# Kernel tuning notes

Hardware: AMD Instinct MI355X
Metric: run time of the kernel (lower is better)

Reference implementation:

```python
import jax, jax.numpy as jnp
import numpy as np

EPS = 1e-5

def _layernorm(x, w, b):
    mu = jnp.mean(x, axis=-1, keepdims=True)
    var = jnp.mean(jnp.square(x - mu), axis=-1, keepdims=True)
    return (x - mu) * jax.lax.rsqrt(var + EPS) * w + b

def setup_inputs() -> dict:
    key = jax.random.key(0)
    ks = jax.random.split(key, 8)
    L, D, FF = 4096, 768, 3072
    s = 1.0 / np.sqrt(D)
    return {
        "x": jax.random.normal(ks[0], (L, D), jnp.float32),
        "in_proj_w": jax.random.normal(ks[1], (3 * D, D), jnp.float32) * s,
        "in_proj_b": jnp.zeros((3 * D,), jnp.float32),
        "out_w": jax.random.normal(ks[2], (D, D), jnp.float32) * s,
        "out_b": jnp.zeros((D,), jnp.float32),
        "ln1_w": jnp.ones((D,), jnp.float32),
        "ln1_b": jnp.zeros((D,), jnp.float32),
        "ln2_w": jnp.ones((D,), jnp.float32),
        "ln2_b": jnp.zeros((D,), jnp.float32),
        "ff_w1": jax.random.normal(ks[3], (FF, D), jnp.float32) * s,
        "ff_b1": jnp.zeros((FF,), jnp.float32),
        "ff_w2": jax.random.normal(ks[4], (D, FF), jnp.float32) * (1.0 / np.sqrt(FF)),
        "ff_b2": jnp.zeros((D,), jnp.float32),
        "window": 128,
    }

def reference(x, in_proj_w, in_proj_b, out_w, out_b, ln1_w, ln1_b, ln2_w, ln2_b, ff_w1, ff_b1, ff_w2, ff_b2, window):
    L, D = x.shape
    H = 12
    hd = D // H
    # packed qkv projection (torch MultiheadAttention in_proj)
    qkv = x @ in_proj_w.T + in_proj_b          # [L, 3D]
    q, k, v = jnp.split(qkv, 3, axis=-1)
    q = q.reshape(L, H, hd).transpose(1, 0, 2)  # [H, L, hd]
    k = k.reshape(L, H, hd).transpose(1, 0, 2)
    v = v.reshape(L, H, hd).transpose(1, 0, 2)
    scores = jnp.einsum('hqd,hkd->hqk', q, k) / np.sqrt(hd)  # [H, L, L]
    idx = jnp.arange(L)
    banned = jnp.abs(idx[:, None] - idx[None, :]) > window    # True = disallowed
    scores = jnp.where(banned[None], -jnp.inf, scores)
    probs = jax.nn.softmax(scores, axis=-1)
    ctx = jnp.einsum('hqk,hkd->hqd', probs, v)               # [H, L, hd]
    ctx = ctx.transpose(1, 0, 2).reshape(L, D)
    attn_out = ctx @ out_w.T + out_b
    h = _layernorm(x + attn_out, ln1_w, ln1_b)
    ff = jax.nn.gelu(h @ ff_w1.T + ff_b1, approximate=False) @ ff_w2.T + ff_b2
    return _layernorm(h + ff, ln2_w, ln2_b)
```

## Files before the change

### kernel.cpp

```cpp
#include <hip/hip_runtime.h>

typedef __bf16 bf16x8 __attribute__((ext_vector_type(8)));
typedef float f32x4 __attribute__((ext_vector_type(4)));

__device__ __forceinline__ unsigned short f2b(float f) {
    unsigned int u = __float_as_uint(f);
    u = (u + 0x7fffu + ((u >> 16) & 1u)) >> 16;
    return (unsigned short)u;
}
__device__ __forceinline__ float b2f(unsigned short v) {
    return __uint_as_float(((unsigned int)v) << 16);
}

__global__ __launch_bounds__(256) void cvt_all(
    const float* __restrict__ s0, unsigned short* __restrict__ d0,
    const float* __restrict__ s1, unsigned short* __restrict__ d1,
    const float* __restrict__ s2, unsigned short* __restrict__ d2,
    const float* __restrict__ s3, unsigned short* __restrict__ d3,
    const float* __restrict__ s4, unsigned short* __restrict__ d4)
{
    int i = blockIdx.x * 256 + threadIdx.x;
    const float* s; unsigned short* d; int j;
    if (i < 786432)       { s = s0; d = d0; j = i; }
    else if (i < 1228800) { s = s1; d = d1; j = i - 786432; }
    else if (i < 1376256) { s = s2; d = d2; j = i - 1228800; }
    else if (i < 1966080) { s = s3; d = d3; j = i - 1376256; }
    else                  { s = s4; d = d4; j = i - 1966080; }
    float4 v = ((const float4*)s)[j];
    ushort4 o;
    o.x = f2b(v.x); o.y = f2b(v.y); o.z = f2b(v.z); o.w = f2b(v.w);
    ((ushort4*)d)[j] = o;
}

#define GL16(g, s) __builtin_amdgcn_global_load_lds( \
    (const __attribute__((address_space(1))) unsigned int*)(g), \
    (__attribute__((address_space(3))) unsigned int*)(s), 16, 0, 0)

template<int EPI>
__global__ __launch_bounds__(256) void gemm128(
    const unsigned short* __restrict__ A,
    const unsigned short* __restrict__ B,
    const float* __restrict__ bias,
    unsigned short* __restrict__ Cb,
    int M, int N, int K)
{
    __shared__ __align__(16) unsigned short As[128 * 64];
    __shared__ __align__(16) unsigned short Bs[128 * 64];
    const int nwg = gridDim.x * gridDim.y;
    const int lin = blockIdx.y * gridDim.x + blockIdx.x;
    const int qq = nwg >> 3;
    const int swz = (lin & 7) * qq + (lin >> 3);
    const int bx = swz % gridDim.x;
    const int by = swz / gridDim.x;

    const int tid = threadIdx.x;
    const int l = tid & 63;
    const int w = tid >> 6;
    const int wr = w >> 1, wc = w & 1;
    const long arow = (long)by * 128 + (tid >> 3);
    const long brow = (long)bx * 128 + (tid >> 3);
    const int kc = (tid & 7) * 8;
    const unsigned short* Ap = A + arow * K + kc;
    const unsigned short* Bp = B + brow * K + kc;

    const int kslice = K / gridDim.z;
    const int kbeg = blockIdx.z * kslice;
    const int kend = kbeg + kslice;

    f32x4 acc[4][4] = {};

    for (int k0 = kbeg; k0 < kend; k0 += 64) {
#pragma unroll
        for (int i = 0; i < 4; ++i) {
            GL16(Ap + k0 + (long)32 * i * K, As + i * 2048 + tid * 8);
            GL16(Bp + k0 + (long)32 * i * K, Bs + i * 2048 + tid * 8);
        }
        __syncthreads();
#pragma unroll
        for (int kk = 0; kk < 2; ++kk) {
            bf16x8 a[4], b[4];
#pragma unroll
            for (int m = 0; m < 4; ++m)
                a[m] = *(const bf16x8*)&As[(wr * 64 + m * 16 + (l & 15)) * 64 + kk * 32 + (l >> 4) * 8];
#pragma unroll
            for (int n = 0; n < 4; ++n)
                b[n] = *(const bf16x8*)&Bs[(wc * 64 + n * 16 + (l & 15)) * 64 + kk * 32 + (l >> 4) * 8];
#pragma unroll
            for (int m = 0; m < 4; ++m)
#pragma unroll
                for (int n = 0; n < 4; ++n)
                    acc[m][n] = __builtin_amdgcn_mfma_f32_16x16x32_bf16(a[m], b[n], acc[m][n], 0, 0, 0);
        }
        __syncthreads();
    }

    const int r0 = by * 128 + wr * 64 + ((l >> 4) << 2);
    const int c0 = bx * 128 + wc * 64 + (l & 15);
#pragma unroll
    for (int n = 0; n < 4; ++n) {
        const int col = c0 + n * 16;
        const float bv = (EPI == 4) ? 0.0f : bias[col];
#pragma unroll
        for (int m = 0; m < 4; ++m) {
#pragma unroll
            for (int r = 0; r < 4; ++r) {
                long row = r0 + m * 16 + r;
                float v = acc[m][n][r];
                if (EPI == 4) {
                    Cb[(long)blockIdx.z * M * N + row * N + col] = f2b(v);
                } else {
                    v += bv;
                    if (EPI == 2) v = 0.5f * v * (1.0f + erff(v * 0.70710678f));
                    Cb[row * N + col] = f2b(v);
                }
            }
        }
    }
}

__global__ __launch_bounds__(256) void attn_local(
    const unsigned short* __restrict__ qkv,
    unsigned short* __restrict__ ctx,
    const int* __restrict__ winp)
{
    const int L = 4096;
    const int W = *winp;
    const int h = blockIdx.y;
    const int q0 = blockIdx.x * 64;
    const int tid = threadIdx.x;
    const int w = tid >> 6, l = tid & 63;
    __shared__ __align__(16) unsigned short Qs[64 * 64];
    __shared__ __align__(16) unsigned short Ks[64 * 64];
    __shared__ __align__(16) unsigned short Vs[64 * 64];
    __shared__ __align__(16) unsigned short Ps[64 * 64];

    {
        const int cg = tid & 7;
#pragma unroll
        for (int i = 0; i < 2; ++i) {
            int r = (tid >> 3) + 32 * i;
            uint4 v = *(const uint4*)&qkv[(long)(q0 + r) * 2304 + h * 64 + cg * 8];
            *(uint4*)&Qs[r * 64 + ((cg ^ (r & 7)) << 3)] = v;
        }
    }

    float mrow[4], lrow[4];
    f32x4 o[4] = {};
#pragma unroll
    for (int r = 0; r < 4; ++r) { mrow[r] = -1e30f; lrow[r] = 0.0f; }

    for (int st = 0; st < 5; ++st) {
        const int k0 = q0 - 128 + st * 64;
        __syncthreads();
        {
            const int cg = tid & 7;
#pragma unroll
            for (int i = 0; i < 2; ++i) {
                int r = (tid >> 3) + 32 * i;
                int kr = k0 + r;
                int krc = kr < 0 ? 0 : (kr >= L ? L - 1 : kr);
                uint4 kv = *(const uint4*)&qkv[(long)krc * 2304 + 768 + h * 64 + cg * 8];
                *(uint4*)&Ks[r * 64 + ((cg ^ (r & 7)) << 3)] = kv;
                uint4 vv = *(const uint4*)&qkv[(long)krc * 2304 + 1536 + h * 64 + cg * 8];
#pragma unroll
                for (int jj = 0; jj < 4; ++jj) {
                    unsigned int word = (jj == 0) ? vv.x : (jj == 1) ? vv.y : (jj == 2) ? vv.z : vv.w;
                    int d0 = cg * 8 + jj * 2;
                    int d1 = d0 + 1;
                    Vs[d0 * 64 + (((r >> 3) ^ (d0 & 7)) << 3) + (r & 7)] = (unsigned short)(word & 0xffffu);
                    Vs[d1 * 64 + (((r >> 3) ^ (d1 & 7)) << 3) + (r & 7)] = (unsigned short)(word >> 16);
                }
            }
        }
        __syncthreads();

        f32x4 s[4] = {};
#pragma unroll
        for (int kk = 0; kk < 2; ++kk) {
            const int aro = w * 16 + (l & 15);
            bf16x8 aq = *(const bf16x8*)&Qs[aro * 64 + (((kk * 4 + (l >> 4)) ^ (aro & 7)) << 3)];
#pragma unroll
            for (int n = 0; n < 4; ++n) {
                const int bro = n * 16 + (l & 15);
                bf16x8 bk = *(const bf16x8*)&Ks[bro * 64 + (((kk * 4 + (l >> 4)) ^ (bro & 7)) << 3)];
                s[n] = __builtin_amdgcn_mfma_f32_16x16x32_bf16(aq, bk, s[n], 0, 0, 0);
            }
        }

        const int qrow = q0 + w * 16 + ((l >> 4) << 2);
        const int kcol = k0 + (l & 15);
        float p[4][4];
#pragma unroll
        for (int n = 0; n < 4; ++n) {
#pragma unroll
            for (int r = 0; r < 4; ++r) {
                int key = kcol + n * 16;
                int q = qrow + r;
                int dd = q - key; if (dd < 0) dd = -dd;
                bool banned = (key < 0) || (key >= L) || (dd > W);
                p[n][r] = banned ? -1e30f : s[n][r] * 0.125f;
            }
        }
        float mx[4];
#pragma unroll
        for (int r = 0; r < 4; ++r)
            mx[r] = fmaxf(fmaxf(p[0][r], p[1][r]), fmaxf(p[2][r], p[3][r]));
#pragma unroll
        for (int off = 8; off >= 1; off >>= 1)
#pragma unroll
            for (int r = 0; r < 4; ++r)
                mx[r] = fmaxf(mx[r], __shfl_xor(mx[r], off));

        float sc[4], mn[4];
#pragma unroll
        for (int r = 0; r < 4; ++r) {
            mn[r] = fmaxf(mrow[r], mx[r]);
            sc[r] = __expf(mrow[r] - mn[r]);
            mrow[r] = mn[r];
        }
        float rs[4] = {0.f, 0.f, 0.f, 0.f};
#pragma unroll
        for (int n = 0; n < 4; ++n)
#pragma unroll
            for (int r = 0; r < 4; ++r) {
                float pv = __expf(p[n][r] - mn[r]);
                p[n][r] = pv;
                rs[r] += pv;
            }
#pragma unroll
        for (int off = 8; off >= 1; off >>= 1)
#pragma unroll
            for (int r = 0; r < 4; ++r)
                rs[r] += __shfl_xor(rs[r], off);
#pragma unroll
        for (int r = 0; r < 4; ++r)
            lrow[r] = lrow[r] * sc[r] + rs[r];
#pragma unroll
        for (int n = 0; n < 4; ++n)
#pragma unroll
            for (int r = 0; r < 4; ++r)
                o[n][r] *= sc[r];

#pragma unroll
        for (int n = 0; n < 4; ++n) {
            int col = n * 16 + (l & 15);
            int cb = col >> 3, ci = col & 7;
#pragma unroll
            for (int r = 0; r < 4; ++r) {
                int rp = w * 16 + ((l >> 4) << 2) + r;
                Ps[rp * 64 + ((cb ^ (rp & 7)) << 3) + ci] = f2b(p[n][r]);
            }
        }
#pragma unroll
        for (int kk = 0; kk < 2; ++kk) {
            const int aro = w * 16 + (l & 15);
            bf16x8 ap = *(const bf16x8*)&Ps[aro * 64 + (((kk * 4 + (l >> 4)) ^ (aro & 7)) << 3)];
#pragma unroll
            for (int n = 0; n < 4; ++n) {
                const int bro = n * 16 + (l & 15);
                bf16x8 bv = *(const bf16x8*)&Vs[bro * 64 + (((kk * 4 + (l >> 4)) ^ (bro & 7)) << 3)];
                o[n] = __builtin_amdgcn_mfma_f32_16x16x32_bf16(ap, bv, o[n], 0, 0, 0);
            }
        }
    }

#pragma unroll
    for (int n = 0; n < 4; ++n) {
        int col = h * 64 + n * 16 + (l & 15);
#pragma unroll
        for (int r = 0; r < 4; ++r) {
            int q = q0 + w * 16 + ((l >> 4) << 2) + r;
            ctx[(long)q * 768 + col] = f2b(o[n][r] / lrow[r]);
        }
    }
}

template<int NS, int BF>
__global__ __launch_bounds__(256) void ln_res2(
    const float* __restrict__ A, const void* __restrict__ partsv,
    const float* __restrict__ pbias,
    const float* __restrict__ w, const float* __restrict__ bb,
    float* __restrict__ outf, unsigned short* __restrict__ outb)
{
    const int D = 768;
    const long PS = (long)4096 * 768;
    const int row = blockIdx.x;
    const int t = threadIdx.x;
    const long base = (long)row * D;
    float xs[3];
#pragma unroll
    for (int i = 0; i < 3; ++i) {
        int c = t + i * 256;
        float v = A[base + c] + pbias[c];
        if (BF) {
            const unsigned short* pb = (const unsigned short*)partsv;
#pragma unroll
            for (int s = 0; s < NS; ++s) v += b2f(pb[s * PS + base + c]);
        } else {
            const float* pf = (const float*)partsv;
#pragma unroll
            for (int s = 0; s < NS; ++s) v += pf[s * PS + base + c];
        }
        xs[i] = v;
    }
    float s = xs[0] + xs[1] + xs[2];
    float ss = xs[0] * xs[0] + xs[1] * xs[1] + xs[2] * xs[2];
#pragma unroll
    for (int off = 32; off >= 1; off >>= 1) {
        s += __shfl_xor(s, off);
        ss += __shfl_xor(ss, off);
    }
    __shared__ float sm[8];
    if ((t & 63) == 0) { sm[t >> 6] = s; sm[(t >> 6) + 4] = ss; }
    __syncthreads();
    s = sm[0] + sm[1] + sm[2] + sm[3];
    ss = sm[4] + sm[5] + sm[6] + sm[7];
    float mu = s * (1.0f / 768.0f);
    float var = ss * (1.0f / 768.0f) - mu * mu;
    float rstd = rsqrtf(var + 1e-5f);
#pragma unroll
    for (int i = 0; i < 3; ++i) {
        int c = t + i * 256;
        float y = (xs[i] - mu) * rstd * w[c] + bb[c];
        outf[base + c] = y;
        if (outb) outb[base + c] = f2b(y);
    }
}

extern "C" void kernel_launch(void* const* d_in, const int* in_sizes, int n_in,
                              void* d_out, int out_size, void* d_ws, size_t ws_size,
                              hipStream_t stream) {
    const float* x   = (const float*)d_in[0];
    const float* ipw = (const float*)d_in[1];
    const float* ipb = (const float*)d_in[2];
    const float* ow  = (const float*)d_in[3];
    const float* ob  = (const float*)d_in[4];
    const float* l1w = (const float*)d_in[5];
    const float* l1b = (const float*)d_in[6];
    const float* l2w = (const float*)d_in[7];
    const float* l2b = (const float*)d_in[8];
    const float* fw1 = (const float*)d_in[9];
    const float* fb1 = (const float*)d_in[10];
    const float* fw2 = (const float*)d_in[11];
    const float* fb2 = (const float*)d_in[12];
    const int*   win = (const int*)d_in[13];

    const int L = 4096, D = 768, TD = 2304, FF = 3072;
    char* p = (char*)d_ws;
    unsigned short* xb   = (unsigned short*)p; p += (size_t)L * D * 2;
    unsigned short* wqkv = (unsigned short*)p; p += (size_t)TD * D * 2;
    unsigned short* wout = (unsigned short*)p; p += (size_t)D * D * 2;
    unsigned short* wf1  = (unsigned short*)p; p += (size_t)FF * D * 2;
    unsigned short* wf2  = (unsigned short*)p; p += (size_t)FF * D * 2;
    unsigned short* ctxb = (unsigned short*)p; p += (size_t)L * D * 2;
    char* partsRaw       = p;                  p += (size_t)2 * L * D * 4;
    float* hf            = (float*)p;          p += (size_t)L * D * 4;
    unsigned short* big  = (unsigned short*)p; p += (size_t)L * FF * 2;
    unsigned short* qkvb = big;
    unsigned short* gb   = big;
    unsigned short* hb   = ctxb;
    unsigned short* partsB = (unsigned short*)partsRaw;

    cvt_all<<<9984, 256, 0, stream>>>(x, xb, ipw, wqkv, ow, wout, fw1, wf1, fw2, wf2);

    gemm128<0><<<dim3(TD / 128, L / 128, 1), 256, 0, stream>>>(xb, wqkv, ipb, qkvb, L, TD, D);
    attn_local<<<dim3(L / 64, 12), 256, 0, stream>>>(qkvb, ctxb, win);
    gemm128<4><<<dim3(D / 128, L / 128, 4), 256, 0, stream>>>(ctxb, wout, nullptr, partsB, L, D, D);
    ln_res2<4, 1><<<L, 256, 0, stream>>>(x, partsB, ob, l1w, l1b, hf, hb);
    gemm128<2><<<dim3(FF / 128, L / 128, 1), 256, 0, stream>>>(hb, wf1, fb1, gb, L, FF, D);
    gemm128<4><<<dim3(D / 128, L / 128, 4), 256, 0, stream>>>(gb, wf2, nullptr, partsB, L, D, FF);
    ln_res2<4, 1><<<L, 256, 0, stream>>>(hf, partsB, fb2, l2w, l2b, (float*)d_out, nullptr);
}
```

Measured before the change: 308.4 us.

## Double-buffer LDS tiles in GEMM to overlap global loads with MFMA

```diff
diff --git a/kernel.cpp b/kernel.cpp
--- a/kernel.cpp
+++ b/kernel.cpp
@@ -44,8 +44,8 @@
     unsigned short* __restrict__ Cb,
     int M, int N, int K)
 {
-    __shared__ __align__(16) unsigned short As[128 * 64];
-    __shared__ __align__(16) unsigned short Bs[128 * 64];
+    __shared__ __align__(16) unsigned short As[2][128 * 64];
+    __shared__ __align__(16) unsigned short Bs[2][128 * 64];
     const int nwg = gridDim.x * gridDim.y;
     const int lin = blockIdx.y * gridDim.x + blockIdx.x;
     const int qq = nwg >> 3;
@@ -65,33 +65,50 @@
 
     const int kslice = K / gridDim.z;
     const int kbeg = blockIdx.z * kslice;
-    const int kend = kbeg + kslice;
+    const int nt = kslice >> 6;
 
     f32x4 acc[4][4] = {};
 
-    for (int k0 = kbeg; k0 < kend; k0 += 64) {
-#pragma unroll
-        for (int i = 0; i < 4; ++i) {
-            GL16(Ap + k0 + (long)32 * i * K, As + i * 2048 + tid * 8);
-            GL16(Bp + k0 + (long)32 * i * K, Bs + i * 2048 + tid * 8);
-        }
-        __syncthreads();
+#pragma unroll
+    for (int i = 0; i < 4; ++i) {
+        GL16(Ap + kbeg + (long)32 * i * K, &As[0][i * 2048 + tid * 8]);
+        GL16(Bp + kbeg + (long)32 * i * K, &Bs[0][i * 2048 + tid * 8]);
+    }
+
+    for (int t = 0; t < nt; ++t) {
+        const int cur = t & 1;
+        if (t + 1 < nt) {
+            const long k0 = kbeg + (long)(t + 1) * 64;
+#pragma unroll
+            for (int i = 0; i < 4; ++i) {
+                GL16(Ap + k0 + (long)32 * i * K, &As[cur ^ 1][i * 2048 + tid * 8]);
+                GL16(Bp + k0 + (long)32 * i * K, &Bs[cur ^ 1][i * 2048 + tid * 8]);
+            }
+            asm volatile("s_waitcnt vmcnt(8)" ::: "memory");
+        } else {
+            asm volatile("s_waitcnt vmcnt(0)" ::: "memory");
+        }
+        __builtin_amdgcn_s_barrier();
+        __builtin_amdgcn_sched_barrier(0);
+
 #pragma unroll
         for (int kk = 0; kk < 2; ++kk) {
             bf16x8 a[4], b[4];
 #pragma unroll
             for (int m = 0; m < 4; ++m)
-                a[m] = *(const bf16x8*)&As[(wr * 64 + m * 16 + (l & 15)) * 64 + kk * 32 + (l >> 4) * 8];
+                a[m] = *(const bf16x8*)&As[cur][(wr * 64 + m * 16 + (l & 15)) * 64 + kk * 32 + (l >> 4) * 8];
 #pragma unroll
             for (int n = 0; n < 4; ++n)
-                b[n] = *(const bf16x8*)&Bs[(wc * 64 + n * 16 + (l & 15)) * 64 + kk * 32 + (l >> 4) * 8];
+                b[n] = *(const bf16x8*)&Bs[cur][(wc * 64 + n * 16 + (l & 15)) * 64 + kk * 32 + (l >> 4) * 8];
 #pragma unroll
             for (int m = 0; m < 4; ++m)
 #pragma unroll
                 for (int n = 0; n < 4; ++n)
                     acc[m][n] = __builtin_amdgcn_mfma_f32_16x16x32_bf16(a[m], b[n], acc[m][n], 0, 0, 0);
         }
-        __syncthreads();
+        asm volatile("s_waitcnt lgkmcnt(0)" ::: "memory");
+        __builtin_amdgcn_sched_barrier(0);
+        __builtin_amdgcn_s_barrier();
     }
 
     const int r0 = by * 128 + wr * 64 + ((l >> 4) << 2);
```

Measured after the change: 305.8 us. About the same (-0.9%).

## Double-buffer GEMM shared tiles with register-staged global prefetch

Applied to the files above, without the earlier changes.

```diff
diff --git a/kernel.cpp b/kernel.cpp
--- a/kernel.cpp
+++ b/kernel.cpp
@@ -32,20 +32,16 @@
     ((ushort4*)d)[j] = o;
 }
 
-#define GL16(g, s) __builtin_amdgcn_global_load_lds( \
-    (const __attribute__((address_space(1))) unsigned int*)(g), \
-    (__attribute__((address_space(3))) unsigned int*)(s), 16, 0, 0)
-
 template<int EPI>
-__global__ __launch_bounds__(256) void gemm128(
+__global__ __launch_bounds__(256) void gemm128r(
     const unsigned short* __restrict__ A,
     const unsigned short* __restrict__ B,
     const float* __restrict__ bias,
     unsigned short* __restrict__ Cb,
     int M, int N, int K)
 {
-    __shared__ __align__(16) unsigned short As[128 * 64];
-    __shared__ __align__(16) unsigned short Bs[128 * 64];
+    __shared__ __align__(16) unsigned short As[2][128 * 64];
+    __shared__ __align__(16) unsigned short Bs[2][128 * 64];
     const int nwg = gridDim.x * gridDim.y;
     const int lin = blockIdx.y * gridDim.x + blockIdx.x;
     const int qq = nwg >> 3;
@@ -65,31 +61,68 @@
 
     const int kslice = K / gridDim.z;
     const int kbeg = blockIdx.z * kslice;
-    const int kend = kbeg + kslice;
+    const int nt = kslice >> 6;
 
     f32x4 acc[4][4] = {};
-
-    for (int k0 = kbeg; k0 < kend; k0 += 64) {
-#pragma unroll
-        for (int i = 0; i < 4; ++i) {
-            GL16(Ap + k0 + (long)32 * i * K, As + i * 2048 + tid * 8);
-            GL16(Bp + k0 + (long)32 * i * K, Bs + i * 2048 + tid * 8);
-        }
-        __syncthreads();
+    uint4 ra0, ra1, ra2, ra3, rb0, rb1, rb2, rb3;
+
+    ra0 = *(const uint4*)(Ap + kbeg);
+    ra1 = *(const uint4*)(Ap + kbeg + (long)32 * K);
+    ra2 = *(const uint4*)(Ap + kbeg + (long)64 * K);
+    ra3 = *(const uint4*)(Ap + kbeg + (long)96 * K);
+    rb0 = *(const uint4*)(Bp + kbeg);
+    rb1 = *(const uint4*)(Bp + kbeg + (long)32 * K);
+    rb2 = *(const uint4*)(Bp + kbeg + (long)64 * K);
+    rb3 = *(const uint4*)(Bp + kbeg + (long)96 * K);
+    *(uint4*)&As[0][0 * 2048 + tid * 8] = ra0;
+    *(uint4*)&As[0][1 * 2048 + tid * 8] = ra1;
+    *(uint4*)&As[0][2 * 2048 + tid * 8] = ra2;
+    *(uint4*)&As[0][3 * 2048 + tid * 8] = ra3;
+    *(uint4*)&Bs[0][0 * 2048 + tid * 8] = rb0;
+    *(uint4*)&Bs[0][1 * 2048 + tid * 8] = rb1;
+    *(uint4*)&Bs[0][2 * 2048 + tid * 8] = rb2;
+    *(uint4*)&Bs[0][3 * 2048 + tid * 8] = rb3;
+    __syncthreads();
+
+    for (int t = 0; t < nt; ++t) {
+        const int cur = t & 1;
+        const bool pre = (t + 1 < nt);
+        if (pre) {
+            const long k0 = kbeg + (long)(t + 1) * 64;
+            ra0 = *(const uint4*)(Ap + k0);
+            ra1 = *(const uint4*)(Ap + k0 + (long)32 * K);
+            ra2 = *(const uint4*)(Ap + k0 + (long)64 * K);
+            ra3 = *(const uint4*)(Ap + k0 + (long)96 * K);
+            rb0 = *(const uint4*)(Bp + k0);
+            rb1 = *(const uint4*)(Bp + k0 + (long)32 * K);
+            rb2 = *(const uint4*)(Bp + k0 + (long)64 * K);
+            rb3 = *(const uint4*)(Bp + k0 + (long)96 * K);
+        }
 #pragma unroll
         for (int kk = 0; kk < 2; ++kk) {
             bf16x8 a[4], b[4];
 #pragma unroll
             for (int m = 0; m < 4; ++m)
-                a[m] = *(const bf16x8*)&As[(wr * 64 + m * 16 + (l & 15)) * 64 + kk * 32 + (l >> 4) * 8];
+                a[m] = *(const bf16x8*)&As[cur][(wr * 64 + m * 16 + (l & 15)) * 64 + kk * 32 + (l >> 4) * 8];
 #pragma unroll
             for (int n = 0; n < 4; ++n)
-                b[n] = *(const bf16x8*)&Bs[(wc * 64 + n * 16 + (l & 15)) * 64 + kk * 32 + (l >> 4) * 8];
+                b[n] = *(const bf16x8*)&Bs[cur][(wc * 64 + n * 16 + (l & 15)) * 64 + kk * 32 + (l >> 4) * 8];
 #pragma unroll
             for (int m = 0; m < 4; ++m)
 #pragma unroll
                 for (int n = 0; n < 4; ++n)
                     acc[m][n] = __builtin_amdgcn_mfma_f32_16x16x32_bf16(a[m], b[n], acc[m][n], 0, 0, 0);
+        }
+        if (pre) {
+            const int nxt = cur ^ 1;
+            *(uint4*)&As[nxt][0 * 2048 + tid * 8] = ra0;
+            *(uint4*)&As[nxt][1 * 2048 + tid * 8] = ra1;
+            *(uint4*)&As[nxt][2 * 2048 + tid * 8] = ra2;
+            *(uint4*)&As[nxt][3 * 2048 + tid * 8] = ra3;
+            *(uint4*)&Bs[nxt][0 * 2048 + tid * 8] = rb0;
+            *(uint4*)&Bs[nxt][1 * 2048 + tid * 8] = rb1;
+            *(uint4*)&Bs[nxt][2 * 2048 + tid * 8] = rb2;
+            *(uint4*)&Bs[nxt][3 * 2048 + tid * 8] = rb3;
         }
         __syncthreads();
     }
@@ -363,11 +396,11 @@
 
     cvt_all<<<9984, 256, 0, stream>>>(x, xb, ipw, wqkv, ow, wout, fw1, wf1, fw2, wf2);
 
-    gemm128<0><<<dim3(TD / 128, L / 128, 1), 256, 0, stream>>>(xb, wqkv, ipb, qkvb, L, TD, D);
+    gemm128r<0><<<dim3(TD / 128, L / 128, 1), 256, 0, stream>>>(xb, wqkv, ipb, qkvb, L, TD, D);
     attn_local<<<dim3(L / 64, 12), 256, 0, stream>>>(qkvb, ctxb, win);
-    gemm128<4><<<dim3(D / 128, L / 128, 4), 256, 0, stream>>>(ctxb, wout, nullptr, partsB, L, D, D);
+    gemm128r<4><<<dim3(D / 128, L / 128, 4), 256, 0, stream>>>(ctxb, wout, nullptr, partsB, L, D, D);
     ln_res2<4, 1><<<L, 256, 0, stream>>>(x, partsB, ob, l1w, l1b, hf, hb);
-    gemm128<2><<<dim3(FF / 128, L / 128, 1), 256, 0, stream>>>(hb, wf1, fb1, gb, L, FF, D);
-    gemm128<4><<<dim3(D / 128, L / 128, 4), 256, 0, stream>>>(gb, wf2, nullptr, partsB, L, D, FF);
+    gemm128r<2><<<dim3(FF / 128, L / 128, 1), 256, 0, stream>>>(hb, wf1, fb1, gb, L, FF, D);
+    gemm128r<4><<<dim3(D / 128, L / 128, 4), 256, 0, stream>>>(gb, wf2, nullptr, partsB, L, D, FF);
     ln_res2<4, 1><<<L, 256, 0, stream>>>(hf, partsB, fb2, l2w, l2b, (float*)d_out, nullptr);
 }
```

Measured after the change: 284.4 us. 1.08x faster.
